# Performance work log

Measured on AMD Instinct MI355X. Metric: run time of the kernel, lower is better.

Reference implementation:

```python
import jax, jax.numpy as jnp
import numpy as np

N = 100000        # nodes
E = 3200000       # edges
IN = 256          # in_feats
H = 8             # num_heads
O = 64            # out_feats
F = 64            # edge_feats
T = 8             # num_etypes

def setup_inputs() -> dict:
    key = jax.random.key(0)
    ks = jax.random.split(key, 10)
    return {
        "feat": jax.random.normal(ks[0], (N, IN), jnp.float32) * 0.1,
        "etype": jax.random.randint(ks[1], (E,), 0, T, jnp.int32),
        "src": jax.random.randint(ks[2], (E,), 0, N, jnp.int32),
        "dst": jax.random.randint(ks[3], (E,), 0, N, jnp.int32),
        "W_fc": jax.random.normal(ks[4], (IN, H * O), jnp.float32) * (1.0 / np.sqrt(IN)),
        "edge_emb": jax.random.normal(ks[5], (T, F), jnp.float32),
        "W_e": jax.random.normal(ks[6], (F, H * F), jnp.float32) * (1.0 / np.sqrt(F)),
        "attn_l": jax.random.normal(ks[7], (H, O), jnp.float32) * 0.1,
        "attn_r": jax.random.normal(ks[8], (H, O), jnp.float32) * 0.1,
        "attn_e": jax.random.normal(ks[9], (H, F), jnp.float32) * 0.1,
    }

def reference(feat, etype, src, dst, W_fc, edge_emb, W_e, attn_l, attn_r, attn_e):
    n = feat.shape[0]
    # node projection + per-head attention logits
    h = (feat @ W_fc).reshape(n, H, O)                      # [N,H,O]
    el = jnp.einsum('nho,ho->nh', h, attn_l)                # [N,H]
    er = jnp.einsum('nho,ho->nh', h, attn_r)                # [N,H]
    # edge-type embedding -> projection -> logit (project the tiny table once, then gather)
    emb_proj = (edge_emb @ W_e).reshape(T, H, F)            # [T,H,F]
    ee = jnp.einsum('thf,hf->th', emb_proj, attn_e)[etype]  # [E,H]
    # u_add_v + edge bias, then ReLU (module's "leaky_relu" is nn.ReLU())
    e = jax.nn.relu(el[src] + er[dst] + ee)                 # [E,H]
    # segment softmax grouped by destination node
    m = jax.ops.segment_max(e, dst, num_segments=n)         # [N,H]
    ex = jnp.exp(e - m[dst])                                # [E,H]
    s = jax.ops.segment_sum(ex, dst, num_segments=n)        # [N,H]
    return ex / s[dst]                                      # [E,H]
```

## Files before the change

### kernel.cpp

```cpp
#include <hip/hip_runtime.h>
#include <math.h>

#define NN 100000
#define NE 3200000
#define INF_ 256
#define NH 8
#define OF 64
#define EF 64
#define NT 8

#define BSH 7
#define BNODES 128
#define NB 782
#define CAPB 4608
#define SPLIT 4
#define EPB 4096

static constexpr size_t WS_AT      = 0;
static constexpr size_t WS_EE      = 4096;
static constexpr size_t WS_EL      = 4160;
static constexpr size_t WS_ERS     = WS_EL + (size_t)NN * 8;
static constexpr size_t WS_CCNT    = WS_ERS + (size_t)NN * 16;
static constexpr size_t WS_PART    = WS_CCNT + NB + 2;

__global__ __launch_bounds__(256) void k_prep_A(const float* __restrict__ W_fc,
                                                const float* __restrict__ attn_l,
                                                const float* __restrict__ attn_r,
                                                float* __restrict__ At,
                                                unsigned* __restrict__ ccnt) {
    int t = blockIdx.x * 256 + threadIdx.x;
    if (t < NB) ccnt[t] = 0u;
    int c = t >> 8;
    int i = t & 255;
    int h = c & 7;
    const float* attn = (c < 8) ? attn_l : attn_r;
    const float* wrow = W_fc + (size_t)i * (NH * OF) + h * OF;
    const float* arow = attn + h * OF;
    float acc = 0.f;
#pragma unroll 8
    for (int o = 0; o < OF; ++o) acc += wrow[o] * arow[o];
    At[c * INF_ + i] = acc;
}

__global__ __launch_bounds__(512) void k_prep_ee(const float* __restrict__ edge_emb,
                                                 const float* __restrict__ W_e,
                                                 const float* __restrict__ attn_e,
                                                 float* __restrict__ ee_tab) {
    __shared__ float B[EF][NH];
    int t = threadIdx.x;
    int g = t >> 3, h = t & 7;
    const float* wrow = W_e + (size_t)g * (NH * EF) + h * EF;
    const float* arow = attn_e + h * EF;
    float acc = 0.f;
#pragma unroll 8
    for (int f = 0; f < EF; ++f) acc += wrow[f] * arow[f];
    B[g][h] = acc;
    __syncthreads();
    if (t < NT * NH) {
        int tt = t >> 3, hh = t & 7;
        float a = 0.f;
#pragma unroll 8
        for (int g2 = 0; g2 < EF; ++g2) a += edge_emb[tt * EF + g2] * B[g2][hh];
        ee_tab[tt * NH + hh] = a;
    }
}

__global__ __launch_bounds__(256) void k_node(const float* __restrict__ feat,
                                              const float* __restrict__ At,
                                              float* __restrict__ el,
                                              float* __restrict__ ers) {
    int n = blockIdx.x * 256 + threadIdx.x;
    if (n >= NN) return;
    const float4* f4 = (const float4*)(feat + (size_t)n * INF_);
    const float4* A4 = (const float4*)At;
    float acc[16];
#pragma unroll
    for (int c = 0; c < 16; ++c) acc[c] = 0.f;
    for (int iq = 0; iq < INF_ / 4; ++iq) {
        float4 f = f4[iq];
#pragma unroll
        for (int c = 0; c < 16; ++c) {
            float4 a = A4[c * 64 + iq];
            acc[c] += f.x * a.x + f.y * a.y + f.z * a.z + f.w * a.w;
        }
    }
    float4* e4 = (float4*)(el + (size_t)n * 8);
    e4[0] = make_float4(acc[0], acc[1], acc[2], acc[3]);
    e4[1] = make_float4(acc[4], acc[5], acc[6], acc[7]);
    float4* r4 = (float4*)(ers + (size_t)n * 16);
    r4[0] = make_float4(acc[8], acc[9], acc[10], acc[11]);
    r4[1] = make_float4(acc[12], acc[13], acc[14], acc[15]);
    r4[2] = make_float4(0.f, 0.f, 0.f, 0.f);
    r4[3] = make_float4(0.f, 0.f, 0.f, 0.f);
}

__global__ __launch_bounds__(256) void k_partition(const int* __restrict__ src,
                                                   const int* __restrict__ dst,
                                                   const int* __restrict__ etype,
                                                   unsigned* __restrict__ ccnt,
                                                   unsigned* __restrict__ part) {
    __shared__ unsigned hist[NB];
    __shared__ unsigned cursor[NB];
    int tid = threadIdx.x;
    size_t base = (size_t)blockIdx.x * EPB;
    unsigned long long rc[16];
    for (int i = tid; i < NB; i += 256) hist[i] = 0u;
    __syncthreads();
#pragma unroll
    for (int k = 0; k < 16; ++k) {
        size_t j = base + (size_t)k * 256 + tid;
        if (j < NE) {
            int dj = dst[j];
            rc[k] = (unsigned long long)(unsigned)src[j]
                  | ((unsigned long long)(unsigned)etype[j] << 17)
                  | ((unsigned long long)(unsigned)dj << 20);
            atomicAdd(&hist[dj >> BSH], 1u);
        } else rc[k] = ~0ull;
    }
    __syncthreads();
    for (int i = tid; i < NB; i += 256) {
        unsigned h = hist[i];
        cursor[i] = h ? atomicAdd(ccnt + i, h) : 0u;
    }
    __syncthreads();
#pragma unroll
    for (int k = 0; k < 16; ++k) {
        if (rc[k] == ~0ull) continue;
        int dj = (int)(rc[k] >> 20);
        int b = dj >> BSH;
        unsigned pos = atomicAdd(&cursor[b], 1u);
        if (pos < CAPB)
            part[(size_t)b * CAPB + pos] =
                (unsigned)(rc[k] & 0xFFFFFull) | ((unsigned)(dj & (BNODES - 1)) << 20);
    }
}

__global__ __launch_bounds__(256) void k_bucket_sum(const unsigned* __restrict__ part,
                                                    const unsigned* __restrict__ ccnt,
                                                    const float* __restrict__ el,
                                                    const float* __restrict__ ers,
                                                    const float* __restrict__ ee_tab,
                                                    float* __restrict__ ers_out) {
    __shared__ float sbin[BNODES * 9];
    int bs = blockIdx.x;
    int b = bs >> 2, c = bs & 3;
    int tid = threadIdx.x;
    int n0 = b << BSH;
    int nn = NN - n0; if (nn > BNODES) nn = BNODES;

    for (int i = tid; i < BNODES * 9; i += 256) sbin[i] = 0.f;
    __syncthreads();

    unsigned cnt = ccnt[b]; if (cnt > CAPB) cnt = CAPB;
    const unsigned* pp = part + (size_t)b * CAPB;
    for (unsigned e = (unsigned)(c * 256 + tid); e < cnt; e += 1024) {
        unsigned rec = pp[e];
        int sj = (int)(rec & 0x1FFFFu);
        int et = (int)((rec >> 17) & 7u);
        int dl = (int)((rec >> 20) & (BNODES - 1));
        const float4* el4 = (const float4*)(el + (size_t)sj * 8);
        const float4* E   = (const float4*)(ers + (size_t)(n0 + dl) * 16);
        const float4* ee4 = (const float4*)(ee_tab + et * NH);
        float4 la = el4[0], lb = el4[1];
        float4 ra = E[0],   rb = E[1];
        float4 ea = ee4[0], eb = ee4[1];
        float* sb = &sbin[dl * 9];
        atomicAdd(&sb[0], __expf(fmaxf(la.x + ra.x + ea.x, 0.f)));
        atomicAdd(&sb[1], __expf(fmaxf(la.y + ra.y + ea.y, 0.f)));
        atomicAdd(&sb[2], __expf(fmaxf(la.z + ra.z + ea.z, 0.f)));
        atomicAdd(&sb[3], __expf(fmaxf(la.w + ra.w + ea.w, 0.f)));
        atomicAdd(&sb[4], __expf(fmaxf(lb.x + rb.x + eb.x, 0.f)));
        atomicAdd(&sb[5], __expf(fmaxf(lb.y + rb.y + eb.y, 0.f)));
        atomicAdd(&sb[6], __expf(fmaxf(lb.z + rb.z + eb.z, 0.f)));
        atomicAdd(&sb[7], __expf(fmaxf(lb.w + rb.w + eb.w, 0.f)));
    }
    __syncthreads();
    for (int i = tid; i < nn * NH; i += 256) {
        int nl = i >> 3, hh = i & 7;
        atomicAdd(&ers_out[(size_t)(n0 + nl) * 16 + 8 + hh], sbin[nl * 9 + hh]);
    }
}

__global__ __launch_bounds__(256) void k_edge_out(const int* __restrict__ src,
                                                  const int* __restrict__ dst,
                                                  const int* __restrict__ etype,
                                                  const float* __restrict__ el,
                                                  const float* __restrict__ ers,
                                                  const float* __restrict__ ee_tab,
                                                  float* __restrict__ out) {
    int j = blockIdx.x * 256 + threadIdx.x;
    if (j >= NE) return;
    int sj = src[j], dj = dst[j], tj = etype[j];
    const float4* el4 = (const float4*)(el + (size_t)sj * 8);
    const float4* E   = (const float4*)(ers + (size_t)dj * 16);
    const float4* ee4 = (const float4*)(ee_tab + tj * NH);
    float4 l0 = el4[0], l1 = el4[1];
    float4 r0 = E[0], r1 = E[1];
    float4 s0 = E[2], s1 = E[3];
    float4 e0 = ee4[0], e1 = ee4[1];
    float4 o0, o1;
    o0.x = __expf(fmaxf(l0.x + r0.x + e0.x, 0.f)) / s0.x;
    o0.y = __expf(fmaxf(l0.y + r0.y + e0.y, 0.f)) / s0.y;
    o0.z = __expf(fmaxf(l0.z + r0.z + e0.z, 0.f)) / s0.z;
    o0.w = __expf(fmaxf(l0.w + r0.w + e0.w, 0.f)) / s0.w;
    o1.x = __expf(fmaxf(l1.x + r1.x + e1.x, 0.f)) / s1.x;
    o1.y = __expf(fmaxf(l1.y + r1.y + e1.y, 0.f)) / s1.y;
    o1.z = __expf(fmaxf(l1.z + r1.z + e1.z, 0.f)) / s1.z;
    o1.w = __expf(fmaxf(l1.w + r1.w + e1.w, 0.f)) / s1.w;
    float4* o4 = (float4*)(out + (size_t)j * NH);
    o4[0] = o0;
    o4[1] = o1;
}

extern "C" void kernel_launch(void* const* d_in, const int* in_sizes, int n_in,
                              void* d_out, int out_size, void* d_ws, size_t ws_size,
                              hipStream_t stream) {
    const float* feat     = (const float*)d_in[0];
    const int*   etype    = (const int*)d_in[1];
    const int*   src      = (const int*)d_in[2];
    const int*   dst      = (const int*)d_in[3];
    const float* W_fc     = (const float*)d_in[4];
    const float* edge_emb = (const float*)d_in[5];
    const float* W_e      = (const float*)d_in[6];
    const float* attn_l   = (const float*)d_in[7];
    const float* attn_r   = (const float*)d_in[8];
    const float* attn_e   = (const float*)d_in[9];

    float*    ws      = (float*)d_ws;
    float*    At      = ws + WS_AT;
    float*    ee_tab  = ws + WS_EE;
    float*    el      = ws + WS_EL;
    float*    ers     = ws + WS_ERS;
    unsigned* ccnt    = (unsigned*)(ws + WS_CCNT);
    unsigned* part    = (unsigned*)(ws + WS_PART);
    float*    out     = (float*)d_out;

    hipLaunchKernelGGL(k_prep_A, dim3(16), dim3(256), 0, stream, W_fc, attn_l, attn_r, At, ccnt);
    hipLaunchKernelGGL(k_prep_ee, dim3(1), dim3(512), 0, stream, edge_emb, W_e, attn_e, ee_tab);
    hipLaunchKernelGGL(k_node, dim3((NN + 255) / 256), dim3(256), 0, stream, feat, At, el, ers);
    hipLaunchKernelGGL(k_partition, dim3((NE + EPB - 1) / EPB), dim3(256), 0, stream,
                       src, dst, etype, ccnt, part);
    hipLaunchKernelGGL(k_bucket_sum, dim3(NB * SPLIT), dim3(256), 0, stream,
                       part, ccnt, el, ers, ee_tab, ers);
    hipLaunchKernelGGL(k_edge_out, dim3((NE + 255) / 256), dim3(256), 0, stream,
                       src, dst, etype, el, ers, ee_tab, out);
}
```

Baseline: 519.6 us.

## Use exact count-scan bucket partition and bucketed output pass with LDS-staged node data

Replaces the fixed-capacity bucket layout with a count pass plus prefix scan, so the partition array is tightly packed, and stores 64-bit records that carry the edge id. The final output kernel now walks the dst buckets instead of the original edge order. It stages per-node er values and reciprocal sums in shared memory, which turns the gathered ers loads and the divides into LDS reads and multiplies. The cost is an extra pass over dst, doubled record size, and scattered 32-byte output writes by edge id.

```diff
diff --git a/kernel.cpp b/kernel.cpp
--- a/kernel.cpp
+++ b/kernel.cpp
@@ -12,16 +12,19 @@
 #define BSH 7
 #define BNODES 128
 #define NB 782
-#define CAPB 4608
 #define SPLIT 4
 #define EPB 4096
 
-static constexpr size_t WS_AT      = 0;
-static constexpr size_t WS_EE      = 4096;
-static constexpr size_t WS_EL      = 4160;
-static constexpr size_t WS_ERS     = WS_EL + (size_t)NN * 8;
-static constexpr size_t WS_CCNT    = WS_ERS + (size_t)NN * 16;
-static constexpr size_t WS_PART    = WS_CCNT + NB + 2;
+typedef unsigned long long u64;
+
+static constexpr size_t WS_AT     = 0;
+static constexpr size_t WS_EE     = 4096;
+static constexpr size_t WS_EL     = 4160;
+static constexpr size_t WS_ERS    = WS_EL + (size_t)NN * 8;
+static constexpr size_t WS_CCNT   = WS_ERS + (size_t)NN * 16;
+static constexpr size_t WS_BASE   = WS_CCNT + NB;
+static constexpr size_t WS_CUR    = WS_BASE + NB + 1;
+static constexpr size_t WS_PART64 = ((WS_CUR + NB + 1) & ~(size_t)1);
 
 __global__ __launch_bounds__(256) void k_prep_A(const float* __restrict__ W_fc,
                                                 const float* __restrict__ attn_l,
@@ -94,16 +97,51 @@
     r4[3] = make_float4(0.f, 0.f, 0.f, 0.f);
 }
 
+__global__ __launch_bounds__(256) void k_count(const int* __restrict__ dst,
+                                               unsigned* __restrict__ ccnt) {
+    __shared__ unsigned hist[NB];
+    int tid = threadIdx.x;
+    size_t base = (size_t)blockIdx.x * EPB;
+    for (int i = tid; i < NB; i += 256) hist[i] = 0u;
+    __syncthreads();
+#pragma unroll
+    for (int k = 0; k < 16; ++k) {
+        size_t j = base + (size_t)k * 256 + tid;
+        if (j < NE) atomicAdd(&hist[dst[j] >> BSH], 1u);
+    }
+    __syncthreads();
+    for (int i = tid; i < NB; i += 256) {
+        unsigned h = hist[i];
+        if (h) atomicAdd(ccnt + i, h);
+    }
+}
+
+__global__ __launch_bounds__(256) void k_scan(const unsigned* __restrict__ ccnt,
+                                              unsigned* __restrict__ base,
+                                              unsigned* __restrict__ cur) {
+    __shared__ unsigned v[NB];
+    int t = threadIdx.x;
+    for (int i = t; i < NB; i += 256) v[i] = ccnt[i];
+    __syncthreads();
+    if (t == 0) {
+        unsigned acc = 0;
+        for (int i = 0; i < NB; ++i) { unsigned c = v[i]; v[i] = acc; acc += c; }
+    }
+    __syncthreads();
+    for (int i = t; i < NB; i += 256) { base[i] = v[i]; cur[i] = v[i]; }
+    if (t == 0) base[NB] = NE;
+}
+
 __global__ __launch_bounds__(256) void k_partition(const int* __restrict__ src,
                                                    const int* __restrict__ dst,
                                                    const int* __restrict__ etype,
-                                                   unsigned* __restrict__ ccnt,
-                                                   unsigned* __restrict__ part) {
+                                                   unsigned* __restrict__ cur,
+                                                   u64* __restrict__ part64) {
     __shared__ unsigned hist[NB];
-    __shared__ unsigned cursor[NB];
+    __shared__ unsigned curs[NB];
     int tid = threadIdx.x;
     size_t base = (size_t)blockIdx.x * EPB;
-    unsigned long long rc[16];
+    u64 rc[16];
     for (int i = tid; i < NB; i += 256) hist[i] = 0u;
     __syncthreads();
 #pragma unroll
@@ -111,16 +149,16 @@
         size_t j = base + (size_t)k * 256 + tid;
         if (j < NE) {
             int dj = dst[j];
-            rc[k] = (unsigned long long)(unsigned)src[j]
-                  | ((unsigned long long)(unsigned)etype[j] << 17)
-                  | ((unsigned long long)(unsigned)dj << 20);
+            rc[k] = (u64)(unsigned)src[j]
+                  | ((u64)(unsigned)etype[j] << 17)
+                  | ((u64)(unsigned)dj << 20);
             atomicAdd(&hist[dj >> BSH], 1u);
         } else rc[k] = ~0ull;
     }
     __syncthreads();
     for (int i = tid; i < NB; i += 256) {
         unsigned h = hist[i];
-        cursor[i] = h ? atomicAdd(ccnt + i, h) : 0u;
+        curs[i] = h ? atomicAdd(cur + i, h) : 0u;
     }
     __syncthreads();
 #pragma unroll
@@ -128,20 +166,23 @@
         if (rc[k] == ~0ull) continue;
         int dj = (int)(rc[k] >> 20);
         int b = dj >> BSH;
-        unsigned pos = atomicAdd(&cursor[b], 1u);
-        if (pos < CAPB)
-            part[(size_t)b * CAPB + pos] =
-                (unsigned)(rc[k] & 0xFFFFFull) | ((unsigned)(dj & (BNODES - 1)) << 20);
-    }
-}
-
-__global__ __launch_bounds__(256) void k_bucket_sum(const unsigned* __restrict__ part,
-                                                    const unsigned* __restrict__ ccnt,
+        unsigned pos = atomicAdd(&curs[b], 1u);
+        unsigned eid = (unsigned)(base + (size_t)k * 256 + tid);
+        part64[pos] = (rc[k] & 0xFFFFFull)
+                    | ((u64)(unsigned)(dj & (BNODES - 1)) << 20)
+                    | ((u64)eid << 27);
+    }
+}
+
+__global__ __launch_bounds__(256) void k_bucket_sum(const u64* __restrict__ part64,
+                                                    const unsigned* __restrict__ base,
                                                     const float* __restrict__ el,
                                                     const float* __restrict__ ers,
                                                     const float* __restrict__ ee_tab,
                                                     float* __restrict__ ers_out) {
     __shared__ float sbin[BNODES * 9];
+    __shared__ float er_l[BNODES * 9];
+    __shared__ float ee_l[NT * NH];
     int bs = blockIdx.x;
     int b = bs >> 2, c = bs & 3;
     int tid = threadIdx.x;
@@ -149,30 +190,32 @@
     int nn = NN - n0; if (nn > BNODES) nn = BNODES;
 
     for (int i = tid; i < BNODES * 9; i += 256) sbin[i] = 0.f;
-    __syncthreads();
-
-    unsigned cnt = ccnt[b]; if (cnt > CAPB) cnt = CAPB;
-    const unsigned* pp = part + (size_t)b * CAPB;
-    for (unsigned e = (unsigned)(c * 256 + tid); e < cnt; e += 1024) {
-        unsigned rec = pp[e];
+    if (tid < NT * NH) ee_l[tid] = ee_tab[tid];
+    for (int i = tid; i < nn * NH; i += 256) {
+        int nl = i >> 3, hh = i & 7;
+        er_l[nl * 9 + hh] = ers[(size_t)(n0 + nl) * 16 + hh];
+    }
+    __syncthreads();
+
+    unsigned lo = base[b], hiB = base[b + 1];
+    for (unsigned e = lo + (unsigned)(c * 256 + tid); e < hiB; e += 1024) {
+        u64 rec = part64[e];
         int sj = (int)(rec & 0x1FFFFu);
         int et = (int)((rec >> 17) & 7u);
         int dl = (int)((rec >> 20) & (BNODES - 1));
         const float4* el4 = (const float4*)(el + (size_t)sj * 8);
-        const float4* E   = (const float4*)(ers + (size_t)(n0 + dl) * 16);
-        const float4* ee4 = (const float4*)(ee_tab + et * NH);
         float4 la = el4[0], lb = el4[1];
-        float4 ra = E[0],   rb = E[1];
-        float4 ea = ee4[0], eb = ee4[1];
+        const float* erp = &er_l[dl * 9];
+        const float* eep = &ee_l[et * 8];
         float* sb = &sbin[dl * 9];
-        atomicAdd(&sb[0], __expf(fmaxf(la.x + ra.x + ea.x, 0.f)));
-        atomicAdd(&sb[1], __expf(fmaxf(la.y + ra.y + ea.y, 0.f)));
-        atomicAdd(&sb[2], __expf(fmaxf(la.z + ra.z + ea.z, 0.f)));
-        atomicAdd(&sb[3], __expf(fmaxf(la.w + ra.w + ea.w, 0.f)));
-        atomicAdd(&sb[4], __expf(fmaxf(lb.x + rb.x + eb.x, 0.f)));
-        atomicAdd(&sb[5], __expf(fmaxf(lb.y + rb.y + eb.y, 0.f)));
-        atomicAdd(&sb[6], __expf(fmaxf(lb.z + rb.z + eb.z, 0.f)));
-        atomicAdd(&sb[7], __expf(fmaxf(lb.w + rb.w + eb.w, 0.f)));
+        atomicAdd(&sb[0], __expf(fmaxf(la.x + erp[0] + eep[0], 0.f)));
+        atomicAdd(&sb[1], __expf(fmaxf(la.y + erp[1] + eep[1], 0.f)));
+        atomicAdd(&sb[2], __expf(fmaxf(la.z + erp[2] + eep[2], 0.f)));
+        atomicAdd(&sb[3], __expf(fmaxf(la.w + erp[3] + eep[3], 0.f)));
+        atomicAdd(&sb[4], __expf(fmaxf(lb.x + erp[4] + eep[4], 0.f)));
+        atomicAdd(&sb[5], __expf(fmaxf(lb.y + erp[5] + eep[5], 0.f)));
+        atomicAdd(&sb[6], __expf(fmaxf(lb.z + erp[6] + eep[6], 0.f)));
+        atomicAdd(&sb[7], __expf(fmaxf(lb.w + erp[7] + eep[7], 0.f)));
     }
     __syncthreads();
     for (int i = tid; i < nn * NH; i += 256) {
@@ -181,35 +224,52 @@
     }
 }
 
-__global__ __launch_bounds__(256) void k_edge_out(const int* __restrict__ src,
-                                                  const int* __restrict__ dst,
-                                                  const int* __restrict__ etype,
-                                                  const float* __restrict__ el,
-                                                  const float* __restrict__ ers,
-                                                  const float* __restrict__ ee_tab,
-                                                  float* __restrict__ out) {
-    int j = blockIdx.x * 256 + threadIdx.x;
-    if (j >= NE) return;
-    int sj = src[j], dj = dst[j], tj = etype[j];
-    const float4* el4 = (const float4*)(el + (size_t)sj * 8);
-    const float4* E   = (const float4*)(ers + (size_t)dj * 16);
-    const float4* ee4 = (const float4*)(ee_tab + tj * NH);
-    float4 l0 = el4[0], l1 = el4[1];
-    float4 r0 = E[0], r1 = E[1];
-    float4 s0 = E[2], s1 = E[3];
-    float4 e0 = ee4[0], e1 = ee4[1];
-    float4 o0, o1;
-    o0.x = __expf(fmaxf(l0.x + r0.x + e0.x, 0.f)) / s0.x;
-    o0.y = __expf(fmaxf(l0.y + r0.y + e0.y, 0.f)) / s0.y;
-    o0.z = __expf(fmaxf(l0.z + r0.z + e0.z, 0.f)) / s0.z;
-    o0.w = __expf(fmaxf(l0.w + r0.w + e0.w, 0.f)) / s0.w;
-    o1.x = __expf(fmaxf(l1.x + r1.x + e1.x, 0.f)) / s1.x;
-    o1.y = __expf(fmaxf(l1.y + r1.y + e1.y, 0.f)) / s1.y;
-    o1.z = __expf(fmaxf(l1.z + r1.z + e1.z, 0.f)) / s1.z;
-    o1.w = __expf(fmaxf(l1.w + r1.w + e1.w, 0.f)) / s1.w;
-    float4* o4 = (float4*)(out + (size_t)j * NH);
-    o4[0] = o0;
-    o4[1] = o1;
+__global__ __launch_bounds__(256) void k_out(const u64* __restrict__ part64,
+                                             const unsigned* __restrict__ base,
+                                             const float* __restrict__ el,
+                                             const float* __restrict__ ers,
+                                             const float* __restrict__ ee_tab,
+                                             float* __restrict__ out) {
+    __shared__ float st[BNODES * 17];
+    __shared__ float ee_l[NT * NH];
+    int bs = blockIdx.x;
+    int b = bs >> 2, c = bs & 3;
+    int tid = threadIdx.x;
+    int n0 = b << BSH;
+    int nn = NN - n0; if (nn > BNODES) nn = BNODES;
+
+    if (tid < NT * NH) ee_l[tid] = ee_tab[tid];
+    for (int i = tid; i < nn * 16; i += 256) {
+        int nl = i >> 4, q = i & 15;
+        float v = ers[(size_t)(n0 + nl) * 16 + q];
+        st[nl * 17 + q] = (q < 8) ? v : 1.0f / v;
+    }
+    __syncthreads();
+
+    unsigned lo = base[b], hiB = base[b + 1];
+    for (unsigned e = lo + (unsigned)(c * 256 + tid); e < hiB; e += 1024) {
+        u64 rec = part64[e];
+        int sj = (int)(rec & 0x1FFFFu);
+        int et = (int)((rec >> 17) & 7u);
+        int dl = (int)((rec >> 20) & (BNODES - 1));
+        unsigned eid = (unsigned)(rec >> 27);
+        const float4* el4 = (const float4*)(el + (size_t)sj * 8);
+        float4 la = el4[0], lb = el4[1];
+        const float* sp = &st[dl * 17];
+        const float* eep = &ee_l[et * 8];
+        float4 o0, o1;
+        o0.x = __expf(fmaxf(la.x + sp[0] + eep[0], 0.f)) * sp[8];
+        o0.y = __expf(fmaxf(la.y + sp[1] + eep[1], 0.f)) * sp[9];
+        o0.z = __expf(fmaxf(la.z + sp[2] + eep[2], 0.f)) * sp[10];
+        o0.w = __expf(fmaxf(la.w + sp[3] + eep[3], 0.f)) * sp[11];
+        o1.x = __expf(fmaxf(lb.x + sp[4] + eep[4], 0.f)) * sp[12];
+        o1.y = __expf(fmaxf(lb.y + sp[5] + eep[5], 0.f)) * sp[13];
+        o1.z = __expf(fmaxf(lb.z + sp[6] + eep[6], 0.f)) * sp[14];
+        o1.w = __expf(fmaxf(lb.w + sp[7] + eep[7], 0.f)) * sp[15];
+        float4* o4 = (float4*)(out + (size_t)eid * 8);
+        o4[0] = o0;
+        o4[1] = o1;
+    }
 }
 
 extern "C" void kernel_launch(void* const* d_in, const int* in_sizes, int n_in,
@@ -232,16 +292,20 @@
     float*    el      = ws + WS_EL;
     float*    ers     = ws + WS_ERS;
     unsigned* ccnt    = (unsigned*)(ws + WS_CCNT);
-    unsigned* part    = (unsigned*)(ws + WS_PART);
+    unsigned* basep   = (unsigned*)(ws + WS_BASE);
+    unsigned* cur     = (unsigned*)(ws + WS_CUR);
+    u64*      part64  = (u64*)(ws + WS_PART64);
     float*    out     = (float*)d_out;
 
     hipLaunchKernelGGL(k_prep_A, dim3(16), dim3(256), 0, stream, W_fc, attn_l, attn_r, At, ccnt);
     hipLaunchKernelGGL(k_prep_ee, dim3(1), dim3(512), 0, stream, edge_emb, W_e, attn_e, ee_tab);
     hipLaunchKernelGGL(k_node, dim3((NN + 255) / 256), dim3(256), 0, stream, feat, At, el, ers);
+    hipLaunchKernelGGL(k_count, dim3((NE + EPB - 1) / EPB), dim3(256), 0, stream, dst, ccnt);
+    hipLaunchKernelGGL(k_scan, dim3(1), dim3(256), 0, stream, ccnt, basep, cur);
     hipLaunchKernelGGL(k_partition, dim3((NE + EPB - 1) / EPB), dim3(256), 0, stream,
-                       src, dst, etype, ccnt, part);
+                       src, dst, etype, cur, part64);
     hipLaunchKernelGGL(k_bucket_sum, dim3(NB * SPLIT), dim3(256), 0, stream,
-                       part, ccnt, el, ers, ee_tab, ers);
-    hipLaunchKernelGGL(k_edge_out, dim3((NE + 255) / 256), dim3(256), 0, stream,
-                       src, dst, etype, el, ers, ee_tab, out);
-}
+                       part64, basep, el, ers, ee_tab, ers);
+    hipLaunchKernelGGL(k_out, dim3(NB * SPLIT), dim3(256), 0, stream,
+                       part64, basep, el, ers, ee_tab, out);
+}
```

New measurement: 594.0 us. +14.3%, slower.
